# Optimization experiments

Hardware: AMD Instinct MI355X
Metric: run time of the kernel (lower is better)

## Reference

```python
import jax, jax.numpy as jnp
import numpy as np
import math

SPARSITY = 0.95


def _linear(x, W, b):
    # torch nn.Linear: y = x @ W.T + b, W is [out, in]
    return jnp.einsum('bsd,od->bso', x, W) + b


def setup_inputs() -> dict:
    key = jax.random.key(0)
    ks = jax.random.split(key, 11)
    B, S, D = 2, 4096, 512
    std = 1.0 / math.sqrt(D)
    inp = {
        'x': jax.random.normal(ks[0], (B, S, D), dtype=jnp.float32),
        'mask_rand': jax.random.uniform(ks[1], (B, S, S), dtype=jnp.float32),
        'Wq': jax.random.normal(ks[2], (D, D), dtype=jnp.float32) * std,
        'bq': jax.random.normal(ks[3], (D,), dtype=jnp.float32) * std,
        'Wk': jax.random.normal(ks[4], (D, D), dtype=jnp.float32) * std,
        'bk': jax.random.normal(ks[5], (D,), dtype=jnp.float32) * std,
        'Wv': jax.random.normal(ks[6], (D, D), dtype=jnp.float32) * std,
        'bv': jax.random.normal(ks[7], (D,), dtype=jnp.float32) * std,
        'Wo': jax.random.normal(ks[8], (D, D), dtype=jnp.float32) * std,
        'bo': jax.random.normal(ks[9], (D,), dtype=jnp.float32) * std,
    }
    return inp


def reference(x, mask_rand, Wq, bq, Wk, bk, Wv, bv, Wo, bo):
    B, S, D = x.shape
    Q = _linear(x, Wq, bq)
    K = _linear(x, Wk, bk)
    V = _linear(x, Wv, bv)
    scores = jnp.einsum('bqd,bkd->bqk', Q, K) / jnp.sqrt(jnp.asarray(D, x.dtype))
    keep = mask_rand > SPARSITY  # random sparsity mask
    sparse_scores = jnp.where(keep, scores, -jnp.inf)
    attn = jax.nn.softmax(sparse_scores, axis=-1)
    attn_out = jnp.einsum('bqk,bkd->bqd', attn, V)
    # faithful to torch: transpose(1,2).contiguous().view(B, S, D)
    attn_out = jnp.swapaxes(attn_out, 1, 2).reshape(B, S, D)
    return _linear(attn_out, Wo, bo)
```

## Files before the change

### kernel.cpp

```cpp
#include <hip/hip_runtime.h>
#include <hip/hip_bf16.h>
#include <math.h>

typedef __bf16 bf16_t;
typedef __attribute__((ext_vector_type(8))) __bf16 bf16x8;
typedef __attribute__((ext_vector_type(4))) float f32x4;

constexpr int B_ = 2, S_ = 4096, D_ = 512;
constexpr int BS_ = B_ * S_;

__device__ __forceinline__ void load16_lds(const bf16_t* g, bf16_t* l) {
    __builtin_amdgcn_global_load_lds(
        (const __attribute__((address_space(1))) void*)g,
        (__attribute__((address_space(3))) void*)l, 16, 0, 0);
}

__global__ __launch_bounds__(256) void cvt_all(
    const float* __restrict__ x, const float* __restrict__ Wq,
    const float* __restrict__ Wk, const float* __restrict__ Wv,
    const float* __restrict__ Wo, bf16_t* __restrict__ dst)
{
    constexpr long QKV = (long)BS_ * D_;
    constexpr long WE  = (long)D_ * D_;
    const long i = ((long)blockIdx.x * 256 + threadIdx.x) * 4;
    const float* src;
    long o;
    if (i < QKV) { src = x; o = i; }
    else {
        const long j = i - QKV;
        const int w = (int)(j >> 18);
        o = j & (WE - 1);
        src = (w == 0) ? Wq : (w == 1) ? Wk : (w == 2) ? Wv : Wo;
    }
    const float4 v = *(const float4*)(src + o);
    bf16_t out[4] = {(bf16_t)v.x, (bf16_t)v.y, (bf16_t)v.z, (bf16_t)v.w};
    *(uint2*)(dst + i) = *(uint2*)out;
}

__global__ __launch_bounds__(256) void pack_mask(
    const float* __restrict__ mask, unsigned char* __restrict__ bm)
{
    const long i = ((long)blockIdx.x * 256 + threadIdx.x) * 16;
    unsigned char o[16];
#pragma unroll
    for (int c = 0; c < 4; c++) {
        const float4 v = *(const float4*)(mask + i + c * 4);
        o[c * 4 + 0] = v.x > 0.95f;
        o[c * 4 + 1] = v.y > 0.95f;
        o[c * 4 + 2] = v.z > 0.95f;
        o[c * 4 + 3] = v.w > 0.95f;
    }
    *(uint4*)(bm + i) = *(uint4*)o;
}

__global__ __launch_bounds__(256) void qkv_gemm(
    const bf16_t* __restrict__ X,
    const bf16_t* __restrict__ Wq, const bf16_t* __restrict__ Wk, const bf16_t* __restrict__ Wv,
    const float* __restrict__ bq, const float* __restrict__ bk, const float* __restrict__ bv,
    bf16_t* __restrict__ Q, bf16_t* __restrict__ Kout, bf16_t* __restrict__ V)
{
    constexpr int K = 512, N = 512;
    const int sel = blockIdx.x >> 2;
    const bf16_t* B = (sel == 0) ? Wq : (sel == 1) ? Wk : Wv;
    const float* bias = (sel == 0) ? bq : (sel == 1) ? bk : bv;
    bf16_t* C = (sel == 0) ? Q : (sel == 1) ? Kout : V;

    __shared__ bf16_t As[128 * 32];
    __shared__ bf16_t Bs[128 * 32];

    const int tid  = threadIdx.x;
    const int wave = tid >> 6;
    const int lane = tid & 63;
    const int quad = lane >> 4;
    const int r16  = lane & 15;
    const int wr   = wave >> 1;
    const int wc   = wave & 1;

    const int m0 = blockIdx.y * 128;
    const int n0 = (blockIdx.x & 3) * 128;

    const int srow = tid >> 2;
    const int scol = (tid & 3) * 8;

    const bf16_t* gA0 = X + (long)(m0 + srow) * K + scol;
    const bf16_t* gA1 = gA0 + (long)64 * K;
    const bf16_t* gB0 = B + (long)(n0 + srow) * K + scol;
    const bf16_t* gB1 = gB0 + (long)64 * K;
    bf16_t* lA = As + tid * 8;
    bf16_t* lB = Bs + tid * 8;

    f32x4 acc[4][4] = {};

    for (int k0 = 0; k0 < K; k0 += 32) {
        load16_lds(gA0 + k0, lA);
        load16_lds(gA1 + k0, lA + 2048);
        load16_lds(gB0 + k0, lB);
        load16_lds(gB1 + k0, lB + 2048);
        __syncthreads();

        bf16x8 af[4], bfr[4];
#pragma unroll
        for (int i = 0; i < 4; i++)
            af[i] = *(const bf16x8*)(As + (wr * 64 + i * 16 + r16) * 32 + quad * 8);
#pragma unroll
        for (int j = 0; j < 4; j++)
            bfr[j] = *(const bf16x8*)(Bs + (wc * 64 + j * 16 + r16) * 32 + quad * 8);

#pragma unroll
        for (int i = 0; i < 4; i++)
#pragma unroll
            for (int j = 0; j < 4; j++)
                acc[i][j] = __builtin_amdgcn_mfma_f32_16x16x32_bf16(af[i], bfr[j], acc[i][j], 0, 0, 0);
        __syncthreads();
    }

#pragma unroll
    for (int i = 0; i < 4; i++) {
#pragma unroll
        for (int j = 0; j < 4; j++) {
            const int gn = n0 + wc * 64 + j * 16 + r16;
            const float bval = bias[gn];
#pragma unroll
            for (int reg = 0; reg < 4; reg++) {
                const int gm = m0 + wr * 64 + i * 16 + quad * 4 + reg;
                C[(long)gm * N + gn] = (bf16_t)(acc[i][j][reg] + bval);
            }
        }
    }
}

template <typename MT>
__global__ __launch_bounds__(256) void scores_gemm(
    const bf16_t* __restrict__ Q, const bf16_t* __restrict__ Km,
    const MT* __restrict__ mask, bf16_t* __restrict__ SC,
    float* __restrict__ rowsum, float scale)
{
    constexpr int S = S_, K = D_;
    const int b = blockIdx.z;
    const bf16_t* A = Q + (long)b * S * K;
    const bf16_t* Bm = Km + (long)b * S * K;

    __shared__ char smem[16384];
    bf16_t* As = (bf16_t*)smem;
    bf16_t* Bs = (bf16_t*)(smem + 8192);

    const int tid  = threadIdx.x;
    const int wave = tid >> 6;
    const int lane = tid & 63;
    const int quad = lane >> 4;
    const int r16  = lane & 15;
    const int wr   = wave >> 1;
    const int wc   = wave & 1;

    const int m0 = blockIdx.y * 128;
    const int n0 = blockIdx.x * 128;

    const int srow = tid >> 2;
    const int scol = (tid & 3) * 8;

    const bf16_t* gA0 = A + (long)(m0 + srow) * K + scol;
    const bf16_t* gA1 = gA0 + (long)64 * K;
    const bf16_t* gB0 = Bm + (long)(n0 + srow) * K + scol;
    const bf16_t* gB1 = gB0 + (long)64 * K;
    bf16_t* lA = As + tid * 8;
    bf16_t* lB = Bs + tid * 8;

    f32x4 acc[4][4] = {};

    for (int k0 = 0; k0 < K; k0 += 32) {
        load16_lds(gA0 + k0, lA);
        load16_lds(gA1 + k0, lA + 2048);
        load16_lds(gB0 + k0, lB);
        load16_lds(gB1 + k0, lB + 2048);
        __syncthreads();

        bf16x8 af[4], bfr[4];
#pragma unroll
        for (int i = 0; i < 4; i++)
            af[i] = *(const bf16x8*)(As + (wr * 64 + i * 16 + r16) * 32 + quad * 8);
#pragma unroll
        for (int j = 0; j < 4; j++)
            bfr[j] = *(const bf16x8*)(Bs + (wc * 64 + j * 16 + r16) * 32 + quad * 8);

#pragma unroll
        for (int i = 0; i < 4; i++)
#pragma unroll
            for (int j = 0; j < 4; j++)
                acc[i][j] = __builtin_amdgcn_mfma_f32_16x16x32_bf16(af[i], bfr[j], acc[i][j], 0, 0, 0);
        __syncthreads();
    }

    float* wlds = (float*)smem + wave * 1024;
    const int erow = lane >> 2;
    const int ecg  = lane & 3;
    const long mbase = (long)b * S * S;

#pragma unroll
    for (int i = 0; i < 4; i++) {
#pragma unroll
        for (int j = 0; j < 4; j++)
#pragma unroll
            for (int reg = 0; reg < 4; reg++)
                wlds[(quad * 4 + reg) * 64 + j * 16 + r16] = acc[i][j][reg];
        __syncthreads();

        float v[16];
#pragma unroll
        for (int c = 0; c < 4; c++) {
            const float4 t = *(const float4*)(wlds + erow * 64 + ecg * 16 + c * 4);
            v[c * 4 + 0] = t.x; v[c * 4 + 1] = t.y;
            v[c * 4 + 2] = t.z; v[c * 4 + 3] = t.w;
        }

        const int gm = m0 + wr * 64 + i * 16 + erow;
        const int gn = n0 + wc * 64 + ecg * 16;

        float e[16];
        if (sizeof(MT) == 1) {
            const uint4 mb = *(const uint4*)((const unsigned char*)mask + mbase + (long)gm * S + gn);
            const unsigned char* mk = (const unsigned char*)&mb;
#pragma unroll
            for (int t = 0; t < 16; t++)
                e[t] = mk[t] ? __expf(v[t] * scale) : 0.f;
        } else {
            const float* mp = (const float*)mask + mbase + (long)gm * S + gn;
#pragma unroll
            for (int c = 0; c < 4; c++) {
                const float4 mk = *(const float4*)(mp + c * 4);
                e[c * 4 + 0] = (mk.x > 0.95f) ? __expf(v[c * 4 + 0] * scale) : 0.f;
                e[c * 4 + 1] = (mk.y > 0.95f) ? __expf(v[c * 4 + 1] * scale) : 0.f;
                e[c * 4 + 2] = (mk.z > 0.95f) ? __expf(v[c * 4 + 2] * scale) : 0.f;
                e[c * 4 + 3] = (mk.w > 0.95f) ? __expf(v[c * 4 + 3] * scale) : 0.f;
            }
        }

        bf16x8 o0, o1;
        float rsum = 0.f;
#pragma unroll
        for (int t = 0; t < 8; t++) {
            rsum += e[t] + e[t + 8];
            o0[t] = (bf16_t)e[t];
            o1[t] = (bf16_t)e[t + 8];
        }
        bf16_t* cp = SC + mbase + (long)gm * S + gn;
        *(bf16x8*)cp       = o0;
        *(bf16x8*)(cp + 8) = o1;

        rsum += __shfl_xor(rsum, 1, 64);
        rsum += __shfl_xor(rsum, 2, 64);
        if (ecg == 0) atomicAdd(&rowsum[b * S + gm], rsum);
        __syncthreads();
    }
}

template <int PMODE, int KS>
__global__ __launch_bounds__(256) void pv_gemm(
    const bf16_t* __restrict__ VT, const bf16_t* __restrict__ SC,
    const float* __restrict__ rowsum, void* __restrict__ outp)
{
    constexpr int S = S_, D = D_;
    constexpr int KC = S / KS;
    const int z  = blockIdx.z;
    const int b  = z / KS;
    const int ks = z % KS;

    const bf16_t* A  = VT + (long)b * D * S;
    const bf16_t* Bm = SC + (long)b * S * S;

    __shared__ bf16_t As[128 * 32];
    __shared__ bf16_t Bs[128 * 32];

    const int tid  = threadIdx.x;
    const int wave = tid >> 6;
    const int lane = tid & 63;
    const int quad = lane >> 4;
    const int r16  = lane & 15;
    const int wr   = wave >> 1;
    const int wc   = wave & 1;

    const int m0 = blockIdx.y * 128;
    const int n0 = blockIdx.x * 128;

    const int srow = tid >> 2;
    const int scol = (tid & 3) * 8;

    const bf16_t* gA0 = A + (long)(m0 + srow) * S + scol;
    const bf16_t* gA1 = gA0 + (long)64 * S;
    const bf16_t* gB0 = Bm + (long)(n0 + srow) * S + scol;
    const bf16_t* gB1 = gB0 + (long)64 * S;
    bf16_t* lA = As + tid * 8;
    bf16_t* lB = Bs + tid * 8;

    f32x4 acc[4][4] = {};

    const int kbeg = ks * KC;
    const int kend = kbeg + KC;
    for (int k0 = kbeg; k0 < kend; k0 += 32) {
        load16_lds(gA0 + k0, lA);
        load16_lds(gA1 + k0, lA + 2048);
        load16_lds(gB0 + k0, lB);
        load16_lds(gB1 + k0, lB + 2048);
        __syncthreads();

        bf16x8 af[4], bfr[4];
#pragma unroll
        for (int i = 0; i < 4; i++)
            af[i] = *(const bf16x8*)(As + (wr * 64 + i * 16 + r16) * 32 + quad * 8);
#pragma unroll
        for (int j = 0; j < 4; j++)
            bfr[j] = *(const bf16x8*)(Bs + (wc * 64 + j * 16 + r16) * 32 + quad * 8);

#pragma unroll
        for (int i = 0; i < 4; i++)
#pragma unroll
            for (int j = 0; j < 4; j++)
                acc[i][j] = __builtin_amdgcn_mfma_f32_16x16x32_bf16(af[i], bfr[j], acc[i][j], 0, 0, 0);
        __syncthreads();
    }

    const long obase = (PMODE == 2) ? (long)b * D * S
                                    : ((long)ks * B_ + b) * (long)D * S;
#pragma unroll
    for (int i = 0; i < 4; i++) {
#pragma unroll
        for (int j = 0; j < 4; j++) {
            const int gn = n0 + wc * 64 + j * 16 + r16;
            float inv = 1.f;
            if (PMODE == 2 || PMODE == 3) inv = 1.f / rowsum[b * S + gn];
#pragma unroll
            for (int reg = 0; reg < 4; reg++) {
                const int gm = m0 + wr * 64 + i * 16 + quad * 4 + reg;
                const long cidx = obase + (long)gm * S + gn;
                const float v = acc[i][j][reg];
                if (PMODE == 0) ((float*)outp)[cidx]  = v;
                if (PMODE == 2) ((bf16_t*)outp)[cidx] = (bf16_t)(v * inv);
                if (PMODE == 3) ((bf16_t*)outp)[cidx] = (bf16_t)(v * inv);
            }
        }
    }
}

template <typename PT, int KS, int NORM>
__global__ __launch_bounds__(256) void reduce_k(
    const PT* __restrict__ part, const float* __restrict__ rowsum,
    bf16_t* __restrict__ T)
{
    constexpr long TOT = (long)B_ * D_ * S_;
    const long i = ((long)blockIdx.x * 256 + threadIdx.x) * 4;
    if (i >= TOT) return;

    float s[4] = {0.f, 0.f, 0.f, 0.f};
#pragma unroll
    for (int ks = 0; ks < KS; ks++) {
        const PT* p = part + ks * TOT + i;
#pragma unroll
        for (int t = 0; t < 4; t++) s[t] += (float)p[t];
    }
    bf16_t o[4];
    if (NORM) {
        const int b = (int)(i / ((long)D_ * S_));
        const int q = (int)(i & (S_ - 1));
        const float4 rs = *(const float4*)(rowsum + b * S_ + q);
        o[0] = (bf16_t)(s[0] / rs.x);
        o[1] = (bf16_t)(s[1] / rs.y);
        o[2] = (bf16_t)(s[2] / rs.z);
        o[3] = (bf16_t)(s[3] / rs.w);
    } else {
        o[0] = (bf16_t)s[0]; o[1] = (bf16_t)s[1];
        o[2] = (bf16_t)s[2]; o[3] = (bf16_t)s[3];
    }
    *(uint2*)(T + i) = *(uint2*)o;
}

__global__ __launch_bounds__(256) void out_gemm(
    const bf16_t* __restrict__ A, const bf16_t* __restrict__ B,
    const float* __restrict__ bias, float* __restrict__ C)
{
    constexpr int N = 512, K = 512;

    __shared__ bf16_t As[128 * 32];
    __shared__ bf16_t Bs[128 * 32];

    const int tid  = threadIdx.x;
    const int wave = tid >> 6;
    const int lane = tid & 63;
    const int quad = lane >> 4;
    const int r16  = lane & 15;
    const int wr   = wave >> 1;
    const int wc   = wave & 1;

    const int m0 = blockIdx.y * 128;
    const int n0 = blockIdx.x * 128;

    const int srow = tid >> 2;
    const int scol = (tid & 3) * 8;

    const bf16_t* gA0 = A + (long)(m0 + srow) * K + scol;
    const bf16_t* gA1 = gA0 + (long)64 * K;
    const bf16_t* gB0 = B + (long)(n0 + srow) * K + scol;
    const bf16_t* gB1 = gB0 + (long)64 * K;
    bf16_t* lA = As + tid * 8;
    bf16_t* lB = Bs + tid * 8;

    f32x4 acc[4][4] = {};

    for (int k0 = 0; k0 < K; k0 += 32) {
        load16_lds(gA0 + k0, lA);
        load16_lds(gA1 + k0, lA + 2048);
        load16_lds(gB0 + k0, lB);
        load16_lds(gB1 + k0, lB + 2048);
        __syncthreads();

        bf16x8 af[4], bfr[4];
#pragma unroll
        for (int i = 0; i < 4; i++)
            af[i] = *(const bf16x8*)(As + (wr * 64 + i * 16 + r16) * 32 + quad * 8);
#pragma unroll
        for (int j = 0; j < 4; j++)
            bfr[j] = *(const bf16x8*)(Bs + (wc * 64 + j * 16 + r16) * 32 + quad * 8);

#pragma unroll
        for (int i = 0; i < 4; i++)
#pragma unroll
            for (int j = 0; j < 4; j++)
                acc[i][j] = __builtin_amdgcn_mfma_f32_16x16x32_bf16(af[i], bfr[j], acc[i][j], 0, 0, 0);
        __syncthreads();
    }

#pragma unroll
    for (int i = 0; i < 4; i++) {
#pragma unroll
        for (int j = 0; j < 4; j++) {
            const int gn = n0 + wc * 64 + j * 16 + r16;
            const float bval = bias[gn];
#pragma unroll
            for (int reg = 0; reg < 4; reg++) {
                const int gm = m0 + wr * 64 + i * 16 + quad * 4 + reg;
                C[(long)gm * N + gn] = acc[i][j][reg] + bval;
            }
        }
    }
}

__global__ __launch_bounds__(256) void transpose_k(
    const bf16_t* __restrict__ in, bf16_t* __restrict__ out, int rows, int cols)
{
    __shared__ bf16_t tile[32][33];
    const int b = blockIdx.z;
    in  += (long)b * rows * cols;
    out += (long)b * rows * cols;
    const int r0 = blockIdx.y * 32;
    const int c0 = blockIdx.x * 32;
    const int tx = threadIdx.x;
    const int ty = threadIdx.y;
#pragma unroll
    for (int i = 0; i < 4; i++)
        tile[ty + 8 * i][tx] = in[(long)(r0 + ty + 8 * i) * cols + c0 + tx];
    __syncthreads();
#pragma unroll
    for (int i = 0; i < 4; i++)
        out[(long)(c0 + ty + 8 * i) * rows + r0 + tx] = tile[tx][ty + 8 * i];
}

extern "C" void kernel_launch(void* const* d_in, const int* in_sizes, int n_in,
                              void* d_out, int out_size, void* d_ws, size_t ws_size,
                              hipStream_t stream)
{
    constexpr int B = B_, S = S_, D = D_;
    constexpr int BS = BS_;
    constexpr long QKV_ELEMS = (long)BS * D;
    constexpr long W_ELEMS   = (long)D * D;
    constexpr long SC_ELEMS  = (long)BS * S;
    constexpr long MASK_N    = (long)BS * S;

    const float* x_raw = (const float*)d_in[0];
    const float* mask  = (const float*)d_in[1];
    const float* Wq    = (const float*)d_in[2];
    const float* bq    = (const float*)d_in[3];
    const float* Wk    = (const float*)d_in[4];
    const float* bk    = (const float*)d_in[5];
    const float* Wv    = (const float*)d_in[6];
    const float* bv    = (const float*)d_in[7];
    const float* Wo    = (const float*)d_in[8];
    const float* bo    = (const float*)d_in[9];

    char* ws = (char*)d_ws;
    bf16_t* SC  = (bf16_t*)ws;                       ws += SC_ELEMS * 2;
    bf16_t* VT  = (bf16_t*)ws;                       ws += QKV_ELEMS * 2;
    bf16_t* Q   = (bf16_t*)ws;                       ws += QKV_ELEMS * 2;
    bf16_t* Kp  = (bf16_t*)ws;                       ws += QKV_ELEMS * 2;
    bf16_t* V   = (bf16_t*)ws;                       ws += QKV_ELEMS * 2;
    bf16_t* T   = V;
    bf16_t* Xc  = (bf16_t*)ws;                       ws += QKV_ELEMS * 2;
    bf16_t* Wqc = (bf16_t*)ws;                       ws += W_ELEMS * 2;
    bf16_t* Wkc = (bf16_t*)ws;                       ws += W_ELEMS * 2;
    bf16_t* Wvc = (bf16_t*)ws;                       ws += W_ELEMS * 2;
    bf16_t* Woc = (bf16_t*)ws;                       ws += W_ELEMS * 2;
    float*  rowsum = (float*)ws;                     ws += (long)BS * 4;
    unsigned char* bmask = (unsigned char*)ws;
    void* part = (void*)ws;
    const size_t used_base = (size_t)(ws - (char*)d_ws);

    constexpr long PART_ELEMS = 4L * B_ * D_ * S_;
    const int path = (ws_size >= used_base + MASK_N) ? 0
                   : (ws_size >= used_base + PART_ELEMS * 4) ? 1 : 2;

    const float scale = 0.044194173824159216f;
    dim3 blk(256);

    cvt_all<<<dim3((int)((QKV_ELEMS + 4 * W_ELEMS) / 1024)), blk, 0, stream>>>(
        x_raw, Wq, Wk, Wv, Wo, Xc);

    if (path == 0)
        pack_mask<<<dim3((int)(MASK_N / 4096)), blk, 0, stream>>>(mask, bmask);

    qkv_gemm<<<dim3(12, 64), blk, 0, stream>>>(Xc, Wqc, Wkc, Wvc, bq, bk, bv, Q, Kp, V);

    transpose_k<<<dim3(D / 32, S / 32, B), dim3(32, 8), 0, stream>>>(V, VT, S, D);

    hipMemsetAsync(rowsum, 0, (long)BS * 4, stream);
    if (path == 0)
        scores_gemm<unsigned char><<<dim3(S / 128, S / 128, B), blk, 0, stream>>>(
            Q, Kp, bmask, SC, rowsum, scale);
    else
        scores_gemm<float><<<dim3(S / 128, S / 128, B), blk, 0, stream>>>(
            Q, Kp, mask, SC, rowsum, scale);

    if (path == 0) {
        pv_gemm<3, 4><<<dim3(S / 128, D / 128, B * 4), blk, 0, stream>>>(VT, SC, rowsum, part);
        reduce_k<bf16_t, 4, 0><<<dim3((int)(QKV_ELEMS / 1024)), blk, 0, stream>>>(
            (const bf16_t*)part, rowsum, T);
    } else if (path == 1) {
        pv_gemm<0, 4><<<dim3(S / 128, D / 128, B * 4), blk, 0, stream>>>(VT, SC, rowsum, part);
        reduce_k<float, 4, 1><<<dim3((int)(QKV_ELEMS / 1024)), blk, 0, stream>>>(
            (const float*)part, rowsum, T);
    } else {
        pv_gemm<2, 1><<<dim3(S / 128, D / 128, B), blk, 0, stream>>>(VT, SC, rowsum, T);
    }

    out_gemm<<<dim3(4, 64), blk, 0, stream>>>(T, Woc, bo, (float*)d_out);
}
```

Before: 394.7 us.

## Fuse scores, masking and PV into a flash-style split-K attention kernel

Replaces the separate scores GEMM (which wrote a bf16 S×S probability matrix) and the PV GEMM with one fused kernel. Each block computes a 64-query by 128-key score tile, applies the float mask and exp in registers, stages P in swizzled LDS, and multiplies it by V^T, split four ways over keys into fp32 partials. A reduction kernel then sums the partials and normalises by the row sums. This removes the mask-packing pass and the large score-matrix round trip through HBM. In exchange the Q tile is reloaded for every key tile, the block count is small (512), and mask reads are uncoalesced scalar loads.

```diff
diff --git a/kernel.cpp b/kernel.cpp
--- a/kernel.cpp
+++ b/kernel.cpp
@@ -37,22 +37,6 @@
     *(uint2*)(dst + i) = *(uint2*)out;
 }
 
-__global__ __launch_bounds__(256) void pack_mask(
-    const float* __restrict__ mask, unsigned char* __restrict__ bm)
-{
-    const long i = ((long)blockIdx.x * 256 + threadIdx.x) * 16;
-    unsigned char o[16];
-#pragma unroll
-    for (int c = 0; c < 4; c++) {
-        const float4 v = *(const float4*)(mask + i + c * 4);
-        o[c * 4 + 0] = v.x > 0.95f;
-        o[c * 4 + 1] = v.y > 0.95f;
-        o[c * 4 + 2] = v.z > 0.95f;
-        o[c * 4 + 3] = v.w > 0.95f;
-    }
-    *(uint4*)(bm + i) = *(uint4*)o;
-}
-
 __global__ __launch_bounds__(256) void qkv_gemm(
     const bf16_t* __restrict__ X,
     const bf16_t* __restrict__ Wq, const bf16_t* __restrict__ Wk, const bf16_t* __restrict__ Wv,
@@ -129,246 +113,175 @@
     }
 }
 
-template <typename MT>
-__global__ __launch_bounds__(256) void scores_gemm(
-    const bf16_t* __restrict__ Q, const bf16_t* __restrict__ Km,
-    const MT* __restrict__ mask, bf16_t* __restrict__ SC,
-    float* __restrict__ rowsum, float scale)
-{
-    constexpr int S = S_, K = D_;
-    const int b = blockIdx.z;
-    const bf16_t* A = Q + (long)b * S * K;
-    const bf16_t* Bm = Km + (long)b * S * K;
-
-    __shared__ char smem[16384];
-    bf16_t* As = (bf16_t*)smem;
-    bf16_t* Bs = (bf16_t*)(smem + 8192);
+__global__ __launch_bounds__(256, 2) void fused_attn(
+    const bf16_t* __restrict__ Q, const bf16_t* __restrict__ Kg,
+    const bf16_t* __restrict__ VT, const float* __restrict__ mask,
+    float* __restrict__ part, float* __restrict__ rowsum, float scale)
+{
+    constexpr int S = S_, D = D_, KS = 4;
+    constexpr int KC = S / KS;
+
+    const int id  = blockIdx.x;
+    const int swz = (id & 7) * 64 + (id >> 3);
+    const int qt  = swz & 63;
+    const int ks  = (swz >> 6) & 3;
+    const int b   = swz >> 8;
+
+    const int q0   = qt * 64;
+    const int kbeg = ks * KC;
+
+    __shared__ bf16_t Ps[64 * 128];
+    __shared__ bf16_t Ss[16384];
+    bf16_t* Qs  = Ss;
+    bf16_t* Kst = Ss + 64 * 32;
+    bf16_t* VTs = Ss;
 
     const int tid  = threadIdx.x;
     const int wave = tid >> 6;
     const int lane = tid & 63;
     const int quad = lane >> 4;
     const int r16  = lane & 15;
-    const int wr   = wave >> 1;
-    const int wc   = wave & 1;
-
-    const int m0 = blockIdx.y * 128;
-    const int n0 = blockIdx.x * 128;
+
+    const bf16_t* Qb  = Q  + ((long)b * S + q0) * D;
+    const bf16_t* Kb  = Kg + (long)b * S * D;
+    const bf16_t* VTb = VT + (long)b * D * S;
+    const float*  Mb  = mask + ((long)b * S + q0) * S;
+
+    f32x4 oacc[4][8] = {};
+    float rs[4][4] = {};
 
     const int srow = tid >> 2;
     const int scol = (tid & 3) * 8;
 
-    const bf16_t* gA0 = A + (long)(m0 + srow) * K + scol;
-    const bf16_t* gA1 = gA0 + (long)64 * K;
-    const bf16_t* gB0 = Bm + (long)(n0 + srow) * K + scol;
-    const bf16_t* gB1 = gB0 + (long)64 * K;
-    bf16_t* lA = As + tid * 8;
-    bf16_t* lB = Bs + tid * 8;
-
-    f32x4 acc[4][4] = {};
-
-    for (int k0 = 0; k0 < K; k0 += 32) {
-        load16_lds(gA0 + k0, lA);
-        load16_lds(gA1 + k0, lA + 2048);
-        load16_lds(gB0 + k0, lB);
-        load16_lds(gB1 + k0, lB + 2048);
+    for (int kt = 0; kt < KC; kt += 128) {
+        const int kg = kbeg + kt;
+
+        f32x4 sacc[4][2] = {};
+        for (int d0 = 0; d0 < D; d0 += 32) {
+            load16_lds(Qb + (long)srow * D + d0 + scol, Qs + tid * 8);
+            load16_lds(Kb + (long)(kg + srow) * D + d0 + scol, Kst + tid * 8);
+            load16_lds(Kb + (long)(kg + 64 + srow) * D + d0 + scol, Kst + 2048 + tid * 8);
+            __syncthreads();
+
+            bf16x8 aq[4], bk[2];
+#pragma unroll
+            for (int qi = 0; qi < 4; qi++)
+                aq[qi] = *(const bf16x8*)(Qs + (qi * 16 + r16) * 32 + quad * 8);
+#pragma unroll
+            for (int kj = 0; kj < 2; kj++)
+                bk[kj] = *(const bf16x8*)(Kst + (wave * 32 + kj * 16 + r16) * 32 + quad * 8);
+
+#pragma unroll
+            for (int qi = 0; qi < 4; qi++)
+#pragma unroll
+                for (int kj = 0; kj < 2; kj++)
+                    sacc[qi][kj] = __builtin_amdgcn_mfma_f32_16x16x32_bf16(
+                        aq[qi], bk[kj], sacc[qi][kj], 0, 0, 0);
+            __syncthreads();
+        }
+
+        float mv[4][2][4];
+#pragma unroll
+        for (int qi = 0; qi < 4; qi++)
+#pragma unroll
+            for (int kj = 0; kj < 2; kj++) {
+                const long mrow = (long)(qi * 16 + quad * 4) * S
+                                + kg + wave * 32 + kj * 16 + r16;
+#pragma unroll
+                for (int reg = 0; reg < 4; reg++)
+                    mv[qi][kj][reg] = Mb[mrow + (long)reg * S];
+            }
+#pragma unroll
+        for (int qi = 0; qi < 4; qi++)
+#pragma unroll
+            for (int kj = 0; kj < 2; kj++)
+#pragma unroll
+                for (int reg = 0; reg < 4; reg++) {
+                    const float e = (mv[qi][kj][reg] > 0.95f)
+                                  ? __expf(sacc[qi][kj][reg] * scale) : 0.f;
+                    rs[qi][reg] += e;
+                    const int q = qi * 16 + quad * 4 + reg;
+                    const int k = wave * 32 + kj * 16 + r16;
+                    Ps[(q * 128 + k) ^ ((q & 7) << 3)] = (bf16_t)e;
+                }
         __syncthreads();
 
-        bf16x8 af[4], bfr[4];
-#pragma unroll
-        for (int i = 0; i < 4; i++)
-            af[i] = *(const bf16x8*)(As + (wr * 64 + i * 16 + r16) * 32 + quad * 8);
-#pragma unroll
-        for (int j = 0; j < 4; j++)
-            bfr[j] = *(const bf16x8*)(Bs + (wc * 64 + j * 16 + r16) * 32 + quad * 8);
-
-#pragma unroll
-        for (int i = 0; i < 4; i++)
-#pragma unroll
-            for (int j = 0; j < 4; j++)
-                acc[i][j] = __builtin_amdgcn_mfma_f32_16x16x32_bf16(af[i], bfr[j], acc[i][j], 0, 0, 0);
-        __syncthreads();
-    }
-
-    float* wlds = (float*)smem + wave * 1024;
-    const int erow = lane >> 2;
-    const int ecg  = lane & 3;
-    const long mbase = (long)b * S * S;
-
-#pragma unroll
-    for (int i = 0; i < 4; i++) {
-#pragma unroll
-        for (int j = 0; j < 4; j++)
-#pragma unroll
-            for (int reg = 0; reg < 4; reg++)
-                wlds[(quad * 4 + reg) * 64 + j * 16 + r16] = acc[i][j][reg];
-        __syncthreads();
-
-        float v[16];
-#pragma unroll
-        for (int c = 0; c < 4; c++) {
-            const float4 t = *(const float4*)(wlds + erow * 64 + ecg * 16 + c * 4);
-            v[c * 4 + 0] = t.x; v[c * 4 + 1] = t.y;
-            v[c * 4 + 2] = t.z; v[c * 4 + 3] = t.w;
-        }
-
-        const int gm = m0 + wr * 64 + i * 16 + erow;
-        const int gn = n0 + wc * 64 + ecg * 16;
-
-        float e[16];
-        if (sizeof(MT) == 1) {
-            const uint4 mb = *(const uint4*)((const unsigned char*)mask + mbase + (long)gm * S + gn);
-            const unsigned char* mk = (const unsigned char*)&mb;
-#pragma unroll
-            for (int t = 0; t < 16; t++)
-                e[t] = mk[t] ? __expf(v[t] * scale) : 0.f;
-        } else {
-            const float* mp = (const float*)mask + mbase + (long)gm * S + gn;
-#pragma unroll
-            for (int c = 0; c < 4; c++) {
-                const float4 mk = *(const float4*)(mp + c * 4);
-                e[c * 4 + 0] = (mk.x > 0.95f) ? __expf(v[c * 4 + 0] * scale) : 0.f;
-                e[c * 4 + 1] = (mk.y > 0.95f) ? __expf(v[c * 4 + 1] * scale) : 0.f;
-                e[c * 4 + 2] = (mk.z > 0.95f) ? __expf(v[c * 4 + 2] * scale) : 0.f;
-                e[c * 4 + 3] = (mk.w > 0.95f) ? __expf(v[c * 4 + 3] * scale) : 0.f;
-            }
-        }
-
-        bf16x8 o0, o1;
-        float rsum = 0.f;
-#pragma unroll
-        for (int t = 0; t < 8; t++) {
-            rsum += e[t] + e[t + 8];
-            o0[t] = (bf16_t)e[t];
-            o1[t] = (bf16_t)e[t + 8];
-        }
-        bf16_t* cp = SC + mbase + (long)gm * S + gn;
-        *(bf16x8*)cp       = o0;
-        *(bf16x8*)(cp + 8) = o1;
-
-        rsum += __shfl_xor(rsum, 1, 64);
-        rsum += __shfl_xor(rsum, 2, 64);
-        if (ecg == 0) atomicAdd(&rowsum[b * S + gm], rsum);
-        __syncthreads();
-    }
-}
-
-template <int PMODE, int KS>
-__global__ __launch_bounds__(256) void pv_gemm(
-    const bf16_t* __restrict__ VT, const bf16_t* __restrict__ SC,
-    const float* __restrict__ rowsum, void* __restrict__ outp)
-{
-    constexpr int S = S_, D = D_;
-    constexpr int KC = S / KS;
-    const int z  = blockIdx.z;
-    const int b  = z / KS;
-    const int ks = z % KS;
-
-    const bf16_t* A  = VT + (long)b * D * S;
-    const bf16_t* Bm = SC + (long)b * S * S;
-
-    __shared__ bf16_t As[128 * 32];
-    __shared__ bf16_t Bs[128 * 32];
-
-    const int tid  = threadIdx.x;
-    const int wave = tid >> 6;
-    const int lane = tid & 63;
-    const int quad = lane >> 4;
-    const int r16  = lane & 15;
-    const int wr   = wave >> 1;
-    const int wc   = wave & 1;
-
-    const int m0 = blockIdx.y * 128;
-    const int n0 = blockIdx.x * 128;
-
-    const int srow = tid >> 2;
-    const int scol = (tid & 3) * 8;
-
-    const bf16_t* gA0 = A + (long)(m0 + srow) * S + scol;
-    const bf16_t* gA1 = gA0 + (long)64 * S;
-    const bf16_t* gB0 = Bm + (long)(n0 + srow) * S + scol;
-    const bf16_t* gB1 = gB0 + (long)64 * S;
-    bf16_t* lA = As + tid * 8;
-    bf16_t* lB = Bs + tid * 8;
-
-    f32x4 acc[4][4] = {};
-
-    const int kbeg = ks * KC;
-    const int kend = kbeg + KC;
-    for (int k0 = kbeg; k0 < kend; k0 += 32) {
-        load16_lds(gA0 + k0, lA);
-        load16_lds(gA1 + k0, lA + 2048);
-        load16_lds(gB0 + k0, lB);
-        load16_lds(gB1 + k0, lB + 2048);
-        __syncthreads();
-
-        bf16x8 af[4], bfr[4];
-#pragma unroll
-        for (int i = 0; i < 4; i++)
-            af[i] = *(const bf16x8*)(As + (wr * 64 + i * 16 + r16) * 32 + quad * 8);
-#pragma unroll
-        for (int j = 0; j < 4; j++)
-            bfr[j] = *(const bf16x8*)(Bs + (wc * 64 + j * 16 + r16) * 32 + quad * 8);
-
-#pragma unroll
-        for (int i = 0; i < 4; i++)
-#pragma unroll
-            for (int j = 0; j < 4; j++)
-                acc[i][j] = __builtin_amdgcn_mfma_f32_16x16x32_bf16(af[i], bfr[j], acc[i][j], 0, 0, 0);
-        __syncthreads();
-    }
-
-    const long obase = (PMODE == 2) ? (long)b * D * S
-                                    : ((long)ks * B_ + b) * (long)D * S;
-#pragma unroll
-    for (int i = 0; i < 4; i++) {
-#pragma unroll
-        for (int j = 0; j < 4; j++) {
-            const int gn = n0 + wc * 64 + j * 16 + r16;
-            float inv = 1.f;
-            if (PMODE == 2 || PMODE == 3) inv = 1.f / rowsum[b * S + gn];
-#pragma unroll
-            for (int reg = 0; reg < 4; reg++) {
-                const int gm = m0 + wr * 64 + i * 16 + quad * 4 + reg;
-                const long cidx = obase + (long)gm * S + gn;
-                const float v = acc[i][j][reg];
-                if (PMODE == 0) ((float*)outp)[cidx]  = v;
-                if (PMODE == 2) ((bf16_t*)outp)[cidx] = (bf16_t)(v * inv);
-                if (PMODE == 3) ((bf16_t*)outp)[cidx] = (bf16_t)(v * inv);
-            }
-        }
-    }
-}
-
-template <typename PT, int KS, int NORM>
-__global__ __launch_bounds__(256) void reduce_k(
-    const PT* __restrict__ part, const float* __restrict__ rowsum,
+        for (int kk = 0; kk < 128; kk += 32) {
+#pragma unroll
+            for (int p = 0; p < 8; p++) {
+                const int r = p * 64 + srow;
+                const int g = (tid & 3) ^ (r & 3);
+                load16_lds(VTb + (long)r * S + kg + kk + g * 8,
+                           VTs + p * 2048 + tid * 8);
+            }
+            __syncthreads();
+
+            bf16x8 ap[4], bv[8];
+#pragma unroll
+            for (int qi = 0; qi < 4; qi++) {
+                const int q = qi * 16 + r16;
+                ap[qi] = *(const bf16x8*)(Ps + ((q * 128 + kk + quad * 8) ^ ((q & 7) << 3)));
+            }
+#pragma unroll
+            for (int dj = 0; dj < 8; dj++) {
+                const int d = wave * 128 + dj * 16 + r16;
+                bv[dj] = *(const bf16x8*)(VTs + d * 32 + ((quad ^ (d & 3)) * 8));
+            }
+#pragma unroll
+            for (int qi = 0; qi < 4; qi++)
+#pragma unroll
+                for (int dj = 0; dj < 8; dj++)
+                    oacc[qi][dj] = __builtin_amdgcn_mfma_f32_16x16x32_bf16(
+                        ap[qi], bv[dj], oacc[qi][dj], 0, 0, 0);
+            __syncthreads();
+        }
+    }
+
+#pragma unroll
+    for (int qi = 0; qi < 4; qi++)
+#pragma unroll
+        for (int reg = 0; reg < 4; reg++) {
+            float v = rs[qi][reg];
+            v += __shfl_xor(v, 1, 64);
+            v += __shfl_xor(v, 2, 64);
+            v += __shfl_xor(v, 4, 64);
+            v += __shfl_xor(v, 8, 64);
+            if (r16 == 0)
+                atomicAdd(&rowsum[b * S + q0 + qi * 16 + quad * 4 + reg], v);
+        }
+
+    float* Pb = part + ((long)ks * B_ + b) * (long)D * S;
+#pragma unroll
+    for (int qi = 0; qi < 4; qi++)
+#pragma unroll
+        for (int dj = 0; dj < 8; dj++) {
+            const int d = wave * 128 + dj * 16 + r16;
+            const int q = q0 + qi * 16 + quad * 4;
+            *(f32x4*)(Pb + (long)d * S + q) = oacc[qi][dj];
+        }
+}
+
+__global__ __launch_bounds__(256) void reduce_norm(
+    const float* __restrict__ part, const float* __restrict__ rowsum,
     bf16_t* __restrict__ T)
 {
     constexpr long TOT = (long)B_ * D_ * S_;
     const long i = ((long)blockIdx.x * 256 + threadIdx.x) * 4;
-    if (i >= TOT) return;
 
     float s[4] = {0.f, 0.f, 0.f, 0.f};
 #pragma unroll
-    for (int ks = 0; ks < KS; ks++) {
-        const PT* p = part + ks * TOT + i;
-#pragma unroll
-        for (int t = 0; t < 4; t++) s[t] += (float)p[t];
-    }
+    for (int ks = 0; ks < 4; ks++) {
+        const float4 p = *(const float4*)(part + ks * TOT + i);
+        s[0] += p.x; s[1] += p.y; s[2] += p.z; s[3] += p.w;
+    }
+    const int b = (int)(i / ((long)D_ * S_));
+    const int q = (int)(i & (S_ - 1));
+    const float4 rsv = *(const float4*)(rowsum + b * S_ + q);
     bf16_t o[4];
-    if (NORM) {
-        const int b = (int)(i / ((long)D_ * S_));
-        const int q = (int)(i & (S_ - 1));
-        const float4 rs = *(const float4*)(rowsum + b * S_ + q);
-        o[0] = (bf16_t)(s[0] / rs.x);
-        o[1] = (bf16_t)(s[1] / rs.y);
-        o[2] = (bf16_t)(s[2] / rs.z);
-        o[3] = (bf16_t)(s[3] / rs.w);
-    } else {
-        o[0] = (bf16_t)s[0]; o[1] = (bf16_t)s[1];
-        o[2] = (bf16_t)s[2]; o[3] = (bf16_t)s[3];
-    }
+    o[0] = (bf16_t)(s[0] / rsv.x);
+    o[1] = (bf16_t)(s[1] / rsv.y);
+    o[2] = (bf16_t)(s[2] / rsv.z);
+    o[3] = (bf16_t)(s[3] / rsv.w);
     *(uint2*)(T + i) = *(uint2*)o;
 }
 
@@ -468,10 +381,9 @@
 {
     constexpr int B = B_, S = S_, D = D_;
     constexpr int BS = BS_;
-    constexpr long QKV_ELEMS = (long)BS * D;
-    constexpr long W_ELEMS   = (long)D * D;
-    constexpr long SC_ELEMS  = (long)BS * S;
-    constexpr long MASK_N    = (long)BS * S;
+    constexpr long QKV_ELEMS  = (long)BS * D;
+    constexpr long W_ELEMS    = (long)D * D;
+    constexpr long PART_ELEMS = 4L * B * D * S;
 
     const float* x_raw = (const float*)d_in[0];
     const float* mask  = (const float*)d_in[1];
@@ -485,7 +397,7 @@
     const float* bo    = (const float*)d_in[9];
 
     char* ws = (char*)d_ws;
-    bf16_t* SC  = (bf16_t*)ws;                       ws += SC_ELEMS * 2;
+    float*  part = (float*)ws;                       ws += PART_ELEMS * 4;
     bf16_t* VT  = (bf16_t*)ws;                       ws += QKV_ELEMS * 2;
     bf16_t* Q   = (bf16_t*)ws;                       ws += QKV_ELEMS * 2;
     bf16_t* Kp  = (bf16_t*)ws;                       ws += QKV_ELEMS * 2;
@@ -497,13 +409,6 @@
     bf16_t* Wvc = (bf16_t*)ws;                       ws += W_ELEMS * 2;
     bf16_t* Woc = (bf16_t*)ws;                       ws += W_ELEMS * 2;
     float*  rowsum = (float*)ws;                     ws += (long)BS * 4;
-    unsigned char* bmask = (unsigned char*)ws;
-    void* part = (void*)ws;
-    const size_t used_base = (size_t)(ws - (char*)d_ws);
-
-    constexpr long PART_ELEMS = 4L * B_ * D_ * S_;
-    const int path = (ws_size >= used_base + MASK_N) ? 0
-                   : (ws_size >= used_base + PART_ELEMS * 4) ? 1 : 2;
 
     const float scale = 0.044194173824159216f;
     dim3 blk(256);
@@ -511,32 +416,14 @@
     cvt_all<<<dim3((int)((QKV_ELEMS + 4 * W_ELEMS) / 1024)), blk, 0, stream>>>(
         x_raw, Wq, Wk, Wv, Wo, Xc);
 
-    if (path == 0)
-        pack_mask<<<dim3((int)(MASK_N / 4096)), blk, 0, stream>>>(mask, bmask);
-
     qkv_gemm<<<dim3(12, 64), blk, 0, stream>>>(Xc, Wqc, Wkc, Wvc, bq, bk, bv, Q, Kp, V);
 
     transpose_k<<<dim3(D / 32, S / 32, B), dim3(32, 8), 0, stream>>>(V, VT, S, D);
 
     hipMemsetAsync(rowsum, 0, (long)BS * 4, stream);
-    if (path == 0)
-        scores_gemm<unsigned char><<<dim3(S / 128, S / 128, B), blk, 0, stream>>>(
-            Q, Kp, bmask, SC, rowsum, scale);
-    else
-        scores_gemm<float><<<dim3(S / 128, S / 128, B), blk, 0, stream>>>(
-            Q, Kp, mask, SC, rowsum, scale);
-
-    if (path == 0) {
-        pv_gemm<3, 4><<<dim3(S / 128, D / 128, B * 4), blk, 0, stream>>>(VT, SC, rowsum, part);
-        reduce_k<bf16_t, 4, 0><<<dim3((int)(QKV_ELEMS / 1024)), blk, 0, stream>>>(
-            (const bf16_t*)part, rowsum, T);
-    } else if (path == 1) {
-        pv_gemm<0, 4><<<dim3(S / 128, D / 128, B * 4), blk, 0, stream>>>(VT, SC, rowsum, part);
-        reduce_k<float, 4, 1><<<dim3((int)(QKV_ELEMS / 1024)), blk, 0, stream>>>(
-            (const float*)part, rowsum, T);
-    } else {
-        pv_gemm<2, 1><<<dim3(S / 128, D / 128, B), blk, 0, stream>>>(VT, SC, rowsum, T);
-    }
+    fused_attn<<<dim3(512), blk, 0, stream>>>(Q, Kp, VT, mask, part, rowsum, scale);
+
+    reduce_norm<<<dim3((int)(QKV_ELEMS / 1024)), blk, 0, stream>>>(part, rowsum, T);
 
     out_gemm<<<dim3(4, 64), blk, 0, stream>>>(T, Woc, bo, (float*)d_out);
 }
```

Measured after the change: 458.9 us. 1.16x slower.
